# Optimization experiments

Hardware: AMD Instinct MI355X
Metric: run time of the kernel (lower is better)

Reference implementation:

```python
import jax, jax.numpy as jnp
import numpy as np

K_TOP = 2  # top-k experts per token (MoE k)


def setup_inputs() -> dict:
    key = jax.random.key(0)
    ks = jax.random.split(key, 4)
    B, D, H, E = 4096, 1024, 2048, 8
    x = jax.random.normal(ks[0], (B, D), dtype=jnp.float32)
    w_gate = jax.random.normal(ks[1], (D, E), dtype=jnp.float32) * 0.02
    W1 = jax.random.normal(ks[2], (E, D, H), dtype=jnp.float32) * (1.0 / np.sqrt(D))
    b1 = jnp.zeros((E, H), dtype=jnp.float32)
    W2 = jax.random.normal(ks[3], (E, H, D), dtype=jnp.float32) * (1.0 / np.sqrt(H))
    b2 = jnp.zeros((E, D), dtype=jnp.float32)
    return {"x": x, "w_gate": w_gate, "W1": W1, "b1": b1, "W2": W2, "b2": b2}


def _top_k_gates(logits, k):
    # noisy_top_k_gating, eval path (noisy_gating=False / train=False):
    # softmax over the top-k logits, scattered back to [B, E]; other gates are 0.
    B, E = logits.shape
    top_logits, top_idx = jax.lax.top_k(logits, k)       # [B, k]
    top_gates = jax.nn.softmax(top_logits, axis=-1)      # [B, k]
    rows = jnp.arange(B)[:, None]
    gates = jnp.zeros((B, E), dtype=logits.dtype).at[rows, top_idx].set(top_gates)
    return gates


def reference(x, w_gate, W1, b1, W2, b2):
    # Gating
    logits = x @ w_gate                                  # [B, E]
    gates = _top_k_gates(logits, K_TOP)                  # [B, E], sparse (top-k nonzero)
    # Experts: MLP(fc1 -> relu -> fc2) per expert. Dense-all-experts form is
    # mathematically identical to dispatch/combine since zero gates contribute 0.
    h = jax.nn.relu(jnp.einsum('bd,edh->beh', x, W1) + b1[None])   # [B, E, H]
    y = jnp.einsum('beh,ehd->bed', h, W2) + b2[None]               # [B, E, D]
    out = jnp.einsum('be,bed->bd', gates, y)                       # gated scatter-combine
    return out
```

## Files before the change

kernel.cpp:

```cpp
#include <hip/hip_runtime.h>

#define B_TOK 4096
#define DDIM  1024
#define HDIM  2048
#define NEXP  8
#define MAXTOK 4096
#define BM 128
#define BN 128
#define BK 32

#define OFF_W1T  0ull
#define OFF_W2T  33554432ull
#define OFF_XB   67108864ull
#define OFF_H    75497472ull
#define OFF_Y    109051904ull
#define OFF_TOK  125829120ull
#define OFF_GATE 125960192ull
#define OFF_PAIR 126091264ull
#define OFF_CNT  126124032ull
#define OFF_OFFS 126124096ull
#define OFF_EIDX (OFF_Y)
#define OFF_GCO  (OFF_Y + 16384ull)

typedef __attribute__((ext_vector_type(4))) float f32x4;
typedef __attribute__((ext_vector_type(8))) short bf16x8;

static __device__ __forceinline__ unsigned short f2bf(float f) {
    unsigned u = __builtin_bit_cast(unsigned, f);
    unsigned r = (u + 0x7FFFu + ((u >> 16) & 1u)) >> 16;
    return (unsigned short)r;
}
static __device__ __forceinline__ float bf2f(unsigned short s) {
    unsigned u = ((unsigned)s) << 16;
    return __builtin_bit_cast(float, u);
}

#define AS1(p) ((const __attribute__((address_space(1))) void*)(p))
#define AS3(p) ((__attribute__((address_space(3))) void*)(p))

__global__ void __launch_bounds__(256) gating_logits_kernel(
    const float* __restrict__ x, const float* __restrict__ wg,
    int* __restrict__ eidx, float* __restrict__ gco, short* __restrict__ Xb) {
    int wave = threadIdx.x >> 6;
    int lane = threadIdx.x & 63;
    int b = blockIdx.x * 4 + wave;
    float acc[NEXP];
#pragma unroll
    for (int e = 0; e < NEXP; e++) acc[e] = 0.f;
    const float* xr = x + (size_t)b * DDIM;
    short* xbr = Xb + (size_t)b * DDIM;
#pragma unroll
    for (int i = 0; i < DDIM / 64; i++) {
        int d = i * 64 + lane;
        float xv = xr[d];
        xbr[d] = (short)f2bf(xv);
        const float4* wrow = (const float4*)(wg + (size_t)d * NEXP);
        float4 w0 = wrow[0], w1 = wrow[1];
        acc[0] += xv * w0.x; acc[1] += xv * w0.y; acc[2] += xv * w0.z; acc[3] += xv * w0.w;
        acc[4] += xv * w1.x; acc[5] += xv * w1.y; acc[6] += xv * w1.z; acc[7] += xv * w1.w;
    }
#pragma unroll
    for (int off = 32; off >= 1; off >>= 1)
#pragma unroll
        for (int e = 0; e < NEXP; e++) acc[e] += __shfl_xor(acc[e], off);
    if (lane == 0) {
        int i1 = 0; float m1 = acc[0];
        for (int e = 1; e < NEXP; e++) if (acc[e] > m1) { m1 = acc[e]; i1 = e; }
        int i2 = (i1 == 0) ? 1 : 0; float m2 = -1e30f;
        for (int e = 0; e < NEXP; e++) { if (e == i1) continue; if (acc[e] > m2) { m2 = acc[e]; i2 = e; } }
        float g1 = 1.f / (1.f + expf(m2 - m1));
        eidx[b] = i1 | (i2 << 16);
        gco[b] = g1;
    }
}

__global__ void __launch_bounds__(256) build_kernel(
    const int* __restrict__ eidx, const float* __restrict__ gco,
    int* __restrict__ counts, int* __restrict__ tok,
    float* __restrict__ gate, int* __restrict__ pair) {
    __shared__ int lhist[NEXP];
    __shared__ int gbase[NEXP];
    int t = threadIdx.x;
    if (t < NEXP) lhist[t] = 0;
    __syncthreads();
    int b = blockIdx.x * 256 + t;
    int ep = eidx[b];
    int e1 = ep & 0xffff, e2 = ep >> 16;
    float g1 = gco[b], g2 = 1.f - g1;
    int l1 = atomicAdd(&lhist[e1], 1);
    int l2 = atomicAdd(&lhist[e2], 1);
    __syncthreads();
    if (t < NEXP) gbase[t] = atomicAdd(&counts[t], lhist[t]);
    __syncthreads();
    int s1 = gbase[e1] + l1, s2 = gbase[e2] + l2;
    tok[e1 * MAXTOK + s1] = b; gate[e1 * MAXTOK + s1] = g1; pair[b * 2 + 0] = e1 * MAXTOK + s1;
    tok[e2 * MAXTOK + s2] = b; gate[e2 * MAXTOK + s2] = g2; pair[b * 2 + 1] = e2 * MAXTOK + s2;
}

__global__ void scan_kernel(const int* __restrict__ counts, int* __restrict__ offs) {
    if (threadIdx.x == 0) {
        int s = 0;
        for (int e = 0; e < NEXP; e++) { offs[e] = s; s += counts[e]; }
    }
}

__global__ void __launch_bounds__(256) tcvt_kernel(const float* __restrict__ src, short* __restrict__ dst,
                                                   int R, int C) {
    __shared__ float tile[64][65];
    int e = blockIdx.z;
    size_t base = (size_t)e * R * C;
    int r0 = blockIdx.y * 64, c0 = blockIdx.x * 64;
    int t = threadIdx.x;
    int rr = t >> 4, c4 = (t & 15) * 4;
    const float* s = src + base + (size_t)r0 * C + c0;
#pragma unroll
    for (int i = 0; i < 4; i++) {
        float4 v = *(const float4*)(s + (size_t)(rr + i * 16) * C + c4);
        tile[rr + i * 16][c4 + 0] = v.x; tile[rr + i * 16][c4 + 1] = v.y;
        tile[rr + i * 16][c4 + 2] = v.z; tile[rr + i * 16][c4 + 3] = v.w;
    }
    __syncthreads();
    short* d = dst + base + (size_t)c0 * R + r0;
    int hr0 = t >> 4, dc = (t & 15) * 4;
#pragma unroll
    for (int i = 0; i < 4; i++) {
        int hr = hr0 + i * 16;
        short4 o;
        o.x = (short)f2bf(tile[dc + 0][hr]); o.y = (short)f2bf(tile[dc + 1][hr]);
        o.z = (short)f2bf(tile[dc + 2][hr]); o.w = (short)f2bf(tile[dc + 3][hr]);
        *(short4*)(d + (size_t)hr * R + dc) = o;
    }
}

__global__ void __launch_bounds__(256) fc1_kernel(
    const short* __restrict__ Xb, const short* __restrict__ W1T, const float* __restrict__ b1,
    short* __restrict__ h, const int* __restrict__ tok,
    const int* __restrict__ counts, const int* __restrict__ offs) {
    int e = blockIdx.z;
    int cnt = counts[e];
    int m0 = blockIdx.y * BM;
    if (m0 >= cnt) return;
    int n0 = blockIdx.x * BN;
    int baseh = offs[e];

    __shared__ short As[2][BM * BK];
    __shared__ short Bs[2][BN * BK];

    int t = threadIdx.x;
    int wave = t >> 6, lane = t & 63;

    const short* asrc[2]; const short* bsrc[2];
#pragma unroll
    for (int i = 0; i < 2; i++) {
        int e0 = wave * 512 + i * 2048 + lane * 8;
        int r = e0 >> 5;
        int q = (e0 >> 3) & 3;
        int cks = ((q ^ (r & 3)) << 3);
        int trow = m0 + r;
        int tid2 = (trow < cnt) ? tok[e * MAXTOK + trow] : 0;
        asrc[i] = Xb + (size_t)tid2 * DDIM + cks;
        bsrc[i] = W1T + ((size_t)e * HDIM + n0 + r) * DDIM + cks;
    }
    int d0 = wave * 512, d1 = wave * 512 + 2048;

    int wr = (wave >> 1) * 64, wc = (wave & 1) * 64;
    f32x4 acc[4][4];
    f32x4 zero = {0.f, 0.f, 0.f, 0.f};
#pragma unroll
    for (int m = 0; m < 4; m++)
#pragma unroll
        for (int n = 0; n < 4; n++) acc[m][n] = zero;

    int qsw = (((lane >> 4) ^ (lane & 3)) << 3);
    int aoff[4], boff[4];
#pragma unroll
    for (int m = 0; m < 4; m++) aoff[m] = (wr + m * 16 + (lane & 15)) * BK + qsw;
#pragma unroll
    for (int n = 0; n < 4; n++) boff[n] = (wc + n * 16 + (lane & 15)) * BK + qsw;

#define STAGE1(buf, k0) do { \
    __builtin_amdgcn_global_load_lds(AS1(asrc[0] + (k0)), AS3(&As[buf][d0]), 16, 0, 0); \
    __builtin_amdgcn_global_load_lds(AS1(asrc[1] + (k0)), AS3(&As[buf][d1]), 16, 0, 0); \
    __builtin_amdgcn_global_load_lds(AS1(bsrc[0] + (k0)), AS3(&Bs[buf][d0]), 16, 0, 0); \
    __builtin_amdgcn_global_load_lds(AS1(bsrc[1] + (k0)), AS3(&Bs[buf][d1]), 16, 0, 0); \
} while (0)

    STAGE1(0, 0);
    __syncthreads();
    int cur = 0;
    const int NT = DDIM / BK;
    for (int kt = 0; kt < NT - 1; ++kt) {
        STAGE1(cur ^ 1, (kt + 1) * BK);
        bf16x8 af[4], bg[4];
#pragma unroll
        for (int m = 0; m < 4; m++) af[m] = *(const bf16x8*)(&As[cur][aoff[m]]);
#pragma unroll
        for (int n = 0; n < 4; n++) bg[n] = *(const bf16x8*)(&Bs[cur][boff[n]]);
        __builtin_amdgcn_s_setprio(1);
#pragma unroll
        for (int m = 0; m < 4; m++)
#pragma unroll
            for (int n = 0; n < 4; n++)
                acc[m][n] = __builtin_amdgcn_mfma_f32_16x16x32_bf16(bg[n], af[m], acc[m][n], 0, 0, 0);
        __builtin_amdgcn_s_setprio(0);
        __syncthreads();
        cur ^= 1;
    }
    {
        bf16x8 af[4], bg[4];
#pragma unroll
        for (int m = 0; m < 4; m++) af[m] = *(const bf16x8*)(&As[cur][aoff[m]]);
#pragma unroll
        for (int n = 0; n < 4; n++) bg[n] = *(const bf16x8*)(&Bs[cur][boff[n]]);
#pragma unroll
        for (int m = 0; m < 4; m++)
#pragma unroll
            for (int n = 0; n < 4; n++)
                acc[m][n] = __builtin_amdgcn_mfma_f32_16x16x32_bf16(bg[n], af[m], acc[m][n], 0, 0, 0);
    }
#undef STAGE1

#pragma unroll
    for (int m = 0; m < 4; m++) {
        int row = m0 + wr + m * 16 + (lane & 15);
        if (row < cnt) {
            size_t rb = (size_t)(baseh + row) * HDIM;
#pragma unroll
            for (int n = 0; n < 4; n++) {
                int colb = n0 + wc + n * 16 + ((lane >> 4) << 2);
                float4 bias = *(const float4*)(b1 + e * HDIM + colb);
                float v0 = acc[m][n][0] + bias.x; v0 = v0 > 0.f ? v0 : 0.f;
                float v1 = acc[m][n][1] + bias.y; v1 = v1 > 0.f ? v1 : 0.f;
                float v2 = acc[m][n][2] + bias.z; v2 = v2 > 0.f ? v2 : 0.f;
                float v3 = acc[m][n][3] + bias.w; v3 = v3 > 0.f ? v3 : 0.f;
                short4 o;
                o.x = (short)f2bf(v0); o.y = (short)f2bf(v1);
                o.z = (short)f2bf(v2); o.w = (short)f2bf(v3);
                *(short4*)(h + rb + colb) = o;
            }
        }
    }
}

__global__ void __launch_bounds__(256) fc2_kernel(
    const short* __restrict__ h, const short* __restrict__ W2T, const float* __restrict__ b2,
    short* __restrict__ ybuf, const int* __restrict__ counts, const int* __restrict__ offs) {
    int e = blockIdx.z;
    int cnt = counts[e];
    int m0 = blockIdx.y * BM;
    if (m0 >= cnt) return;
    int n0 = blockIdx.x * BN;
    int baseh = offs[e];

    __shared__ short As[2][BM * BK];
    __shared__ short Bs[2][BN * BK];

    int t = threadIdx.x;
    int wave = t >> 6, lane = t & 63;

    const short* asrc[2]; const short* bsrc[2];
#pragma unroll
    for (int i = 0; i < 2; i++) {
        int e0 = wave * 512 + i * 2048 + lane * 8;
        int r = e0 >> 5;
        int q = (e0 >> 3) & 3;
        int cks = ((q ^ (r & 3)) << 3);
        asrc[i] = h + (size_t)(baseh + m0 + r) * HDIM + cks;
        bsrc[i] = W2T + ((size_t)e * DDIM + n0 + r) * HDIM + cks;
    }
    int d0 = wave * 512, d1 = wave * 512 + 2048;

    int wr = (wave >> 1) * 64, wc = (wave & 1) * 64;
    f32x4 acc[4][4];
    f32x4 zero = {0.f, 0.f, 0.f, 0.f};
#pragma unroll
    for (int m = 0; m < 4; m++)
#pragma unroll
        for (int n = 0; n < 4; n++) acc[m][n] = zero;

    int qsw = (((lane >> 4) ^ (lane & 3)) << 3);
    int aoff[4], boff[4];
#pragma unroll
    for (int m = 0; m < 4; m++) aoff[m] = (wr + m * 16 + (lane & 15)) * BK + qsw;
#pragma unroll
    for (int n = 0; n < 4; n++) boff[n] = (wc + n * 16 + (lane & 15)) * BK + qsw;

#define STAGE2(buf, k0) do { \
    __builtin_amdgcn_global_load_lds(AS1(asrc[0] + (k0)), AS3(&As[buf][d0]), 16, 0, 0); \
    __builtin_amdgcn_global_load_lds(AS1(asrc[1] + (k0)), AS3(&As[buf][d1]), 16, 0, 0); \
    __builtin_amdgcn_global_load_lds(AS1(bsrc[0] + (k0)), AS3(&Bs[buf][d0]), 16, 0, 0); \
    __builtin_amdgcn_global_load_lds(AS1(bsrc[1] + (k0)), AS3(&Bs[buf][d1]), 16, 0, 0); \
} while (0)

    STAGE2(0, 0);
    __syncthreads();
    int cur = 0;
    const int NT = HDIM / BK;
    for (int kt = 0; kt < NT - 1; ++kt) {
        STAGE2(cur ^ 1, (kt + 1) * BK);
        bf16x8 af[4], bg[4];
#pragma unroll
        for (int m = 0; m < 4; m++) af[m] = *(const bf16x8*)(&As[cur][aoff[m]]);
#pragma unroll
        for (int n = 0; n < 4; n++) bg[n] = *(const bf16x8*)(&Bs[cur][boff[n]]);
        __builtin_amdgcn_s_setprio(1);
#pragma unroll
        for (int m = 0; m < 4; m++)
#pragma unroll
            for (int n = 0; n < 4; n++)
                acc[m][n] = __builtin_amdgcn_mfma_f32_16x16x32_bf16(bg[n], af[m], acc[m][n], 0, 0, 0);
        __builtin_amdgcn_s_setprio(0);
        __syncthreads();
        cur ^= 1;
    }
    {
        bf16x8 af[4], bg[4];
#pragma unroll
        for (int m = 0; m < 4; m++) af[m] = *(const bf16x8*)(&As[cur][aoff[m]]);
#pragma unroll
        for (int n = 0; n < 4; n++) bg[n] = *(const bf16x8*)(&Bs[cur][boff[n]]);
#pragma unroll
        for (int m = 0; m < 4; m++)
#pragma unroll
            for (int n = 0; n < 4; n++)
                acc[m][n] = __builtin_amdgcn_mfma_f32_16x16x32_bf16(bg[n], af[m], acc[m][n], 0, 0, 0);
    }
#undef STAGE2

#pragma unroll
    for (int m = 0; m < 4; m++) {
        int row = m0 + wr + m * 16 + (lane & 15);
        if (row < cnt) {
            size_t rb = (size_t)(baseh + row) * DDIM;
#pragma unroll
            for (int n = 0; n < 4; n++) {
                int colb = n0 + wc + n * 16 + ((lane >> 4) << 2);
                float4 bias = *(const float4*)(b2 + e * DDIM + colb);
                short4 o;
                o.x = (short)f2bf(acc[m][n][0] + bias.x);
                o.y = (short)f2bf(acc[m][n][1] + bias.y);
                o.z = (short)f2bf(acc[m][n][2] + bias.z);
                o.w = (short)f2bf(acc[m][n][3] + bias.w);
                *(short4*)(ybuf + rb + colb) = o;
            }
        }
    }
}

__global__ void __launch_bounds__(256) combine_kernel(
    const short* __restrict__ ybuf, const float* __restrict__ gate,
    const int* __restrict__ pair, const int* __restrict__ offs, float* __restrict__ out) {
    int b = blockIdx.x;
    int p0 = pair[b * 2], p1 = pair[b * 2 + 1];
    float g0 = gate[p0], g1 = gate[p1];
    int r0 = offs[p0 >> 12] + (p0 & 4095);
    int r1 = offs[p1 >> 12] + (p1 & 4095);
    const short4* y0 = (const short4*)(ybuf + (size_t)r0 * DDIM);
    const short4* y1 = (const short4*)(ybuf + (size_t)r1 * DDIM);
    float4* o = (float4*)(out + (size_t)b * DDIM);
    int t = threadIdx.x;
    short4 a = y0[t], c = y1[t];
    float4 v;
    v.x = g0 * bf2f((unsigned short)a.x) + g1 * bf2f((unsigned short)c.x);
    v.y = g0 * bf2f((unsigned short)a.y) + g1 * bf2f((unsigned short)c.y);
    v.z = g0 * bf2f((unsigned short)a.z) + g1 * bf2f((unsigned short)c.z);
    v.w = g0 * bf2f((unsigned short)a.w) + g1 * bf2f((unsigned short)c.w);
    o[t] = v;
}

extern "C" void kernel_launch(void* const* d_in, const int* in_sizes, int n_in,
                              void* d_out, int out_size, void* d_ws, size_t ws_size,
                              hipStream_t stream) {
    const float* x  = (const float*)d_in[0];
    const float* wg = (const float*)d_in[1];
    const float* W1 = (const float*)d_in[2];
    const float* b1 = (const float*)d_in[3];
    const float* W2 = (const float*)d_in[4];
    const float* b2 = (const float*)d_in[5];
    float* out = (float*)d_out;
    char* ws = (char*)d_ws;

    short* W1T = (short*)(ws + OFF_W1T);
    short* W2T = (short*)(ws + OFF_W2T);
    short* Xb  = (short*)(ws + OFF_XB);
    short* h   = (short*)(ws + OFF_H);
    short* ybuf = (short*)(ws + OFF_Y);
    int* tok   = (int*)(ws + OFF_TOK);
    float* gate = (float*)(ws + OFF_GATE);
    int* pair  = (int*)(ws + OFF_PAIR);
    int* counts = (int*)(ws + OFF_CNT);
    int* offs  = (int*)(ws + OFF_OFFS);
    int* eidx  = (int*)(ws + OFF_EIDX);
    float* gco = (float*)(ws + OFF_GCO);

    hipMemsetAsync(counts, 0, 64, stream);
    gating_logits_kernel<<<B_TOK / 4, 256, 0, stream>>>(x, wg, eidx, gco, Xb);
    build_kernel<<<B_TOK / 256, 256, 0, stream>>>(eidx, gco, counts, tok, gate, pair);
    scan_kernel<<<1, 64, 0, stream>>>(counts, offs);
    tcvt_kernel<<<dim3(HDIM / 64, DDIM / 64, NEXP), 256, 0, stream>>>(W1, W1T, DDIM, HDIM);
    tcvt_kernel<<<dim3(DDIM / 64, HDIM / 64, NEXP), 256, 0, stream>>>(W2, W2T, HDIM, DDIM);
    fc1_kernel<<<dim3(HDIM / BN, MAXTOK / BM, NEXP), 256, 0, stream>>>(Xb, W1T, b1, h, tok, counts, offs);
    fc2_kernel<<<dim3(DDIM / BN, MAXTOK / BM, NEXP), 256, 0, stream>>>(h, W2T, b2, ybuf, counts, offs);
    combine_kernel<<<B_TOK, 256, 0, stream>>>(ybuf, gate, pair, offs, out);
}
```

Measured before the change: 201.8 us.

## Use 512-thread blocks with BK=64 single-buffered tiles in expert GEMMs

Reworks both expert GEMM kernels to use 8 waves per block, each computing a 64x32 sub-tile, with a K step of 64 and an 8-way XOR swizzle. LDS double buffering is dropped: every K step loads into one buffer, synchronizes, computes and synchronizes again. The intent is more waves per CU and half as many K iterations so that occupancy hides load latency. The cost is that global loads no longer overlap MFMA work within a block, and each wave reuses fewer fragments per LDS read.

Measured after the change: 194.8 us. -3.5%, faster.

```diff
diff --git a/kernel.cpp b/kernel.cpp
--- a/kernel.cpp
+++ b/kernel.cpp
@@ -7,7 +7,7 @@
 #define MAXTOK 4096
 #define BM 128
 #define BN 128
-#define BK 32
+#define BK 64
 
 #define OFF_W1T  0ull
 #define OFF_W2T  33554432ull
@@ -132,7 +132,7 @@
     }
 }
 
-__global__ void __launch_bounds__(256) fc1_kernel(
+__global__ void __launch_bounds__(512, 4) fc1_kernel(
     const short* __restrict__ Xb, const short* __restrict__ W1T, const float* __restrict__ b1,
     short* __restrict__ h, const int* __restrict__ tok,
     const int* __restrict__ counts, const int* __restrict__ offs) {
@@ -143,91 +143,82 @@
     int n0 = blockIdx.x * BN;
     int baseh = offs[e];
 
-    __shared__ short As[2][BM * BK];
-    __shared__ short Bs[2][BN * BK];
+    __shared__ short As[BM * BK];
+    __shared__ short Bs[BN * BK];
 
     int t = threadIdx.x;
     int wave = t >> 6, lane = t & 63;
 
     const short* asrc[2]; const short* bsrc[2];
+    int dsto[2];
 #pragma unroll
     for (int i = 0; i < 2; i++) {
-        int e0 = wave * 512 + i * 2048 + lane * 8;
-        int r = e0 >> 5;
-        int q = (e0 >> 3) & 3;
-        int cks = ((q ^ (r & 3)) << 3);
+        int G = i * 512 + t;
+        int r = G >> 3, q = G & 7;
+        int cks = ((q ^ (r & 7)) << 3);
         int trow = m0 + r;
         int tid2 = (trow < cnt) ? tok[e * MAXTOK + trow] : 0;
         asrc[i] = Xb + (size_t)tid2 * DDIM + cks;
         bsrc[i] = W1T + ((size_t)e * HDIM + n0 + r) * DDIM + cks;
-    }
-    int d0 = wave * 512, d1 = wave * 512 + 2048;
-
-    int wr = (wave >> 1) * 64, wc = (wave & 1) * 64;
-    f32x4 acc[4][4];
+        dsto[i] = G * 8;
+    }
+
+    int wr = wave >> 2, wc = wave & 3;
+    f32x4 acc[4][2];
     f32x4 zero = {0.f, 0.f, 0.f, 0.f};
 #pragma unroll
     for (int m = 0; m < 4; m++)
 #pragma unroll
-        for (int n = 0; n < 4; n++) acc[m][n] = zero;
-
-    int qsw = (((lane >> 4) ^ (lane & 3)) << 3);
-    int aoff[4], boff[4];
-#pragma unroll
-    for (int m = 0; m < 4; m++) aoff[m] = (wr + m * 16 + (lane & 15)) * BK + qsw;
-#pragma unroll
-    for (int n = 0; n < 4; n++) boff[n] = (wc + n * 16 + (lane & 15)) * BK + qsw;
-
-#define STAGE1(buf, k0) do { \
-    __builtin_amdgcn_global_load_lds(AS1(asrc[0] + (k0)), AS3(&As[buf][d0]), 16, 0, 0); \
-    __builtin_amdgcn_global_load_lds(AS1(asrc[1] + (k0)), AS3(&As[buf][d1]), 16, 0, 0); \
-    __builtin_amdgcn_global_load_lds(AS1(bsrc[0] + (k0)), AS3(&Bs[buf][d0]), 16, 0, 0); \
-    __builtin_amdgcn_global_load_lds(AS1(bsrc[1] + (k0)), AS3(&Bs[buf][d1]), 16, 0, 0); \
-} while (0)
-
-    STAGE1(0, 0);
-    __syncthreads();
-    int cur = 0;
+        for (int n = 0; n < 2; n++) acc[m][n] = zero;
+
+    int l15 = lane & 15, l7 = lane & 7, lhi = lane >> 4;
+    int aoff[4][2], boff[2][2];
+#pragma unroll
+    for (int ks = 0; ks < 2; ks++) {
+        int q = (lhi + ks * 4) ^ l7;
+#pragma unroll
+        for (int m = 0; m < 4; m++) aoff[m][ks] = (wr * 64 + m * 16 + l15) * BK + (q << 3);
+#pragma unroll
+        for (int n = 0; n < 2; n++) boff[n][ks] = (wc * 32 + n * 16 + l15) * BK + (q << 3);
+    }
+
     const int NT = DDIM / BK;
-    for (int kt = 0; kt < NT - 1; ++kt) {
-        STAGE1(cur ^ 1, (kt + 1) * BK);
-        bf16x8 af[4], bg[4];
-#pragma unroll
-        for (int m = 0; m < 4; m++) af[m] = *(const bf16x8*)(&As[cur][aoff[m]]);
-#pragma unroll
-        for (int n = 0; n < 4; n++) bg[n] = *(const bf16x8*)(&Bs[cur][boff[n]]);
+    for (int kt = 0; kt < NT; ++kt) {
+        int k0 = kt * BK;
+#pragma unroll
+        for (int i = 0; i < 2; i++) {
+            __builtin_amdgcn_global_load_lds(AS1(asrc[i] + k0), AS3(&As[dsto[i]]), 16, 0, 0);
+            __builtin_amdgcn_global_load_lds(AS1(bsrc[i] + k0), AS3(&Bs[dsto[i]]), 16, 0, 0);
+        }
+        __syncthreads();
+        bf16x8 af[4][2], bg[2][2];
+#pragma unroll
+        for (int ks = 0; ks < 2; ks++) {
+#pragma unroll
+            for (int m = 0; m < 4; m++) af[m][ks] = *(const bf16x8*)(&As[aoff[m][ks]]);
+#pragma unroll
+            for (int n = 0; n < 2; n++) bg[n][ks] = *(const bf16x8*)(&Bs[boff[n][ks]]);
+        }
         __builtin_amdgcn_s_setprio(1);
 #pragma unroll
-        for (int m = 0; m < 4; m++)
-#pragma unroll
-            for (int n = 0; n < 4; n++)
-                acc[m][n] = __builtin_amdgcn_mfma_f32_16x16x32_bf16(bg[n], af[m], acc[m][n], 0, 0, 0);
+        for (int ks = 0; ks < 2; ks++)
+#pragma unroll
+            for (int m = 0; m < 4; m++)
+#pragma unroll
+                for (int n = 0; n < 2; n++)
+                    acc[m][n] = __builtin_amdgcn_mfma_f32_16x16x32_bf16(bg[n][ks], af[m][ks], acc[m][n], 0, 0, 0);
         __builtin_amdgcn_s_setprio(0);
         __syncthreads();
-        cur ^= 1;
-    }
-    {
-        bf16x8 af[4], bg[4];
-#pragma unroll
-        for (int m = 0; m < 4; m++) af[m] = *(const bf16x8*)(&As[cur][aoff[m]]);
-#pragma unroll
-        for (int n = 0; n < 4; n++) bg[n] = *(const bf16x8*)(&Bs[cur][boff[n]]);
-#pragma unroll
-        for (int m = 0; m < 4; m++)
-#pragma unroll
-            for (int n = 0; n < 4; n++)
-                acc[m][n] = __builtin_amdgcn_mfma_f32_16x16x32_bf16(bg[n], af[m], acc[m][n], 0, 0, 0);
-    }
-#undef STAGE1
+    }
 
 #pragma unroll
     for (int m = 0; m < 4; m++) {
-        int row = m0 + wr + m * 16 + (lane & 15);
+        int row = m0 + wr * 64 + m * 16 + l15;
         if (row < cnt) {
             size_t rb = (size_t)(baseh + row) * HDIM;
 #pragma unroll
-            for (int n = 0; n < 4; n++) {
-                int colb = n0 + wc + n * 16 + ((lane >> 4) << 2);
+            for (int n = 0; n < 2; n++) {
+                int colb = n0 + wc * 32 + n * 16 + (lhi << 2);
                 float4 bias = *(const float4*)(b1 + e * HDIM + colb);
                 float v0 = acc[m][n][0] + bias.x; v0 = v0 > 0.f ? v0 : 0.f;
                 float v1 = acc[m][n][1] + bias.y; v1 = v1 > 0.f ? v1 : 0.f;
@@ -242,7 +233,7 @@
     }
 }
 
-__global__ void __launch_bounds__(256) fc2_kernel(
+__global__ void __launch_bounds__(512, 4) fc2_kernel(
     const short* __restrict__ h, const short* __restrict__ W2T, const float* __restrict__ b2,
     short* __restrict__ ybuf, const int* __restrict__ counts, const int* __restrict__ offs) {
     int e = blockIdx.z;
@@ -252,89 +243,80 @@
     int n0 = blockIdx.x * BN;
     int baseh = offs[e];
 
-    __shared__ short As[2][BM * BK];
-    __shared__ short Bs[2][BN * BK];
+    __shared__ short As[BM * BK];
+    __shared__ short Bs[BN * BK];
 
     int t = threadIdx.x;
     int wave = t >> 6, lane = t & 63;
 
     const short* asrc[2]; const short* bsrc[2];
+    int dsto[2];
 #pragma unroll
     for (int i = 0; i < 2; i++) {
-        int e0 = wave * 512 + i * 2048 + lane * 8;
-        int r = e0 >> 5;
-        int q = (e0 >> 3) & 3;
-        int cks = ((q ^ (r & 3)) << 3);
+        int G = i * 512 + t;
+        int r = G >> 3, q = G & 7;
+        int cks = ((q ^ (r & 7)) << 3);
         asrc[i] = h + (size_t)(baseh + m0 + r) * HDIM + cks;
         bsrc[i] = W2T + ((size_t)e * DDIM + n0 + r) * HDIM + cks;
-    }
-    int d0 = wave * 512, d1 = wave * 512 + 2048;
-
-    int wr = (wave >> 1) * 64, wc = (wave & 1) * 64;
-    f32x4 acc[4][4];
+        dsto[i] = G * 8;
+    }
+
+    int wr = wave >> 2, wc = wave & 3;
+    f32x4 acc[4][2];
     f32x4 zero = {0.f, 0.f, 0.f, 0.f};
 #pragma unroll
     for (int m = 0; m < 4; m++)
 #pragma unroll
-        for (int n = 0; n < 4; n++) acc[m][n] = zero;
-
-    int qsw = (((lane >> 4) ^ (lane & 3)) << 3);
-    int aoff[4], boff[4];
-#pragma unroll
-    for (int m = 0; m < 4; m++) aoff[m] = (wr + m * 16 + (lane & 15)) * BK + qsw;
-#pragma unroll
-    for (int n = 0; n < 4; n++) boff[n] = (wc + n * 16 + (lane & 15)) * BK + qsw;
-
-#define STAGE2(buf, k0) do { \
-    __builtin_amdgcn_global_load_lds(AS1(asrc[0] + (k0)), AS3(&As[buf][d0]), 16, 0, 0); \
-    __builtin_amdgcn_global_load_lds(AS1(asrc[1] + (k0)), AS3(&As[buf][d1]), 16, 0, 0); \
-    __builtin_amdgcn_global_load_lds(AS1(bsrc[0] + (k0)), AS3(&Bs[buf][d0]), 16, 0, 0); \
-    __builtin_amdgcn_global_load_lds(AS1(bsrc[1] + (k0)), AS3(&Bs[buf][d1]), 16, 0, 0); \
-} while (0)
-
-    STAGE2(0, 0);
-    __syncthreads();
-    int cur = 0;
+        for (int n = 0; n < 2; n++) acc[m][n] = zero;
+
+    int l15 = lane & 15, l7 = lane & 7, lhi = lane >> 4;
+    int aoff[4][2], boff[2][2];
+#pragma unroll
+    for (int ks = 0; ks < 2; ks++) {
+        int q = (lhi + ks * 4) ^ l7;
+#pragma unroll
+        for (int m = 0; m < 4; m++) aoff[m][ks] = (wr * 64 + m * 16 + l15) * BK + (q << 3);
+#pragma unroll
+        for (int n = 0; n < 2; n++) boff[n][ks] = (wc * 32 + n * 16 + l15) * BK + (q << 3);
+    }
+
     const int NT = HDIM / BK;
-    for (int kt = 0; kt < NT - 1; ++kt) {
-        STAGE2(cur ^ 1, (kt + 1) * BK);
-        bf16x8 af[4], bg[4];
-#pragma unroll
-        for (int m = 0; m < 4; m++) af[m] = *(const bf16x8*)(&As[cur][aoff[m]]);
-#pragma unroll
-        for (int n = 0; n < 4; n++) bg[n] = *(const bf16x8*)(&Bs[cur][boff[n]]);
+    for (int kt = 0; kt < NT; ++kt) {
+        int k0 = kt * BK;
+#pragma unroll
+        for (int i = 0; i < 2; i++) {
+            __builtin_amdgcn_global_load_lds(AS1(asrc[i] + k0), AS3(&As[dsto[i]]), 16, 0, 0);
+            __builtin_amdgcn_global_load_lds(AS1(bsrc[i] + k0), AS3(&Bs[dsto[i]]), 16, 0, 0);
+        }
+        __syncthreads();
+        bf16x8 af[4][2], bg[2][2];
+#pragma unroll
+        for (int ks = 0; ks < 2; ks++) {
+#pragma unroll
+            for (int m = 0; m < 4; m++) af[m][ks] = *(const bf16x8*)(&As[aoff[m][ks]]);
+#pragma unroll
+            for (int n = 0; n < 2; n++) bg[n][ks] = *(const bf16x8*)(&Bs[boff[n][ks]]);
+        }
         __builtin_amdgcn_s_setprio(1);
 #pragma unroll
-        for (int m = 0; m < 4; m++)
-#pragma unroll
-            for (int n = 0; n < 4; n++)
-                acc[m][n] = __builtin_amdgcn_mfma_f32_16x16x32_bf16(bg[n], af[m], acc[m][n], 0, 0, 0);
+        for (int ks = 0; ks < 2; ks++)
+#pragma unroll
+            for (int m = 0; m < 4; m++)
+#pragma unroll
+                for (int n = 0; n < 2; n++)
+                    acc[m][n] = __builtin_amdgcn_mfma_f32_16x16x32_bf16(bg[n][ks], af[m][ks], acc[m][n], 0, 0, 0);
         __builtin_amdgcn_s_setprio(0);
         __syncthreads();
-        cur ^= 1;
-    }
-    {
-        bf16x8 af[4], bg[4];
-#pragma unroll
-        for (int m = 0; m < 4; m++) af[m] = *(const bf16x8*)(&As[cur][aoff[m]]);
-#pragma unroll
-        for (int n = 0; n < 4; n++) bg[n] = *(const bf16x8*)(&Bs[cur][boff[n]]);
-#pragma unroll
-        for (int m = 0; m < 4; m++)
-#pragma unroll
-            for (int n = 0; n < 4; n++)
-                acc[m][n] = __builtin_amdgcn_mfma_f32_16x16x32_bf16(bg[n], af[m], acc[m][n], 0, 0, 0);
-    }
-#undef STAGE2
+    }
 
 #pragma unroll
     for (int m = 0; m < 4; m++) {
-        int row = m0 + wr + m * 16 + (lane & 15);
+        int row = m0 + wr * 64 + m * 16 + l15;
         if (row < cnt) {
             size_t rb = (size_t)(baseh + row) * DDIM;
 #pragma unroll
-            for (int n = 0; n < 4; n++) {
-                int colb = n0 + wc + n * 16 + ((lane >> 4) << 2);
+            for (int n = 0; n < 2; n++) {
+                int colb = n0 + wc * 32 + n * 16 + (lhi << 2);
                 float4 bias = *(const float4*)(b2 + e * DDIM + colb);
                 short4 o;
                 o.x = (short)f2bf(acc[m][n][0] + bias.x);
@@ -399,7 +381,7 @@
     scan_kernel<<<1, 64, 0, stream>>>(counts, offs);
     tcvt_kernel<<<dim3(HDIM / 64, DDIM / 64, NEXP), 256, 0, stream>>>(W1, W1T, DDIM, HDIM);
     tcvt_kernel<<<dim3(DDIM / 64, HDIM / 64, NEXP), 256, 0, stream>>>(W2, W2T, HDIM, DDIM);
-    fc1_kernel<<<dim3(HDIM / BN, MAXTOK / BM, NEXP), 256, 0, stream>>>(Xb, W1T, b1, h, tok, counts, offs);
-    fc2_kernel<<<dim3(DDIM / BN, MAXTOK / BM, NEXP), 256, 0, stream>>>(h, W2T, b2, ybuf, counts, offs);
+    fc1_kernel<<<dim3(HDIM / BN, MAXTOK / BM, NEXP), 512, 0, stream>>>(Xb, W1T, b1, h, tok, counts, offs);
+    fc2_kernel<<<dim3(DDIM / BN, MAXTOK / BM, NEXP), 512, 0, stream>>>(h, W2T, b2, ybuf, counts, offs);
     combine_kernel<<<B_TOK, 256, 0, stream>>>(ybuf, gate, pair, offs, out);
 }
```
